# Optimization experiments

Measured on AMD Instinct MI355X. Metric: run time of the kernel, lower is better.

Reference implementation:

```python
import jax, jax.numpy as jnp
import numpy as np

NP = 16  # num_patches per side (init kwarg)


def setup_inputs() -> dict:
    key = jax.random.key(0)
    ks = jax.random.split(key, 8)
    B, C, H, W = 16, 16, 256, 256
    ph, pw = H // NP, W // NP          # 16, 16
    D = C * ph * pw                     # in_channels = 4096
    E = 512                             # embedding_dim
    s = 0.02
    return {
        "x": jax.random.normal(ks[0], (B, C, H, W), dtype=jnp.float32),
        "theta_w": jax.random.normal(ks[1], (D, E), dtype=jnp.float32) * s,
        "theta_b": jnp.zeros((E,), dtype=jnp.float32),
        "f_w": jax.random.normal(ks[2], (D, E), dtype=jnp.float32) * s,
        "f_b": jnp.zeros((E,), dtype=jnp.float32),
        "g_w": jax.random.normal(ks[3], (D, D), dtype=jnp.float32) * s,
        "g_b": jnp.zeros((D,), dtype=jnp.float32),
        "scale": jnp.ones((1,), dtype=jnp.float32),
    }


def reference(x, theta_w, theta_b, f_w, f_b, g_w, g_b, scale):
    B, C, H, W = x.shape
    ph, pw = H // NP, W // NP
    P = NP * NP                 # number of patches (== ph*pw by construction)
    D = C * ph * pw             # flattened patch dim = in_channels
    # extract non-overlapping patches: [B,C,H,W] -> [B,P,D] (C,ph,pw order)
    p = (x.reshape(B, C, NP, ph, NP, pw)
           .transpose(0, 2, 4, 1, 3, 5)
           .reshape(B, P, D))
    theta = p @ theta_w + theta_b                         # [B,P,E]
    f = p @ f_w + f_b                                     # [B,P,E]
    weights = jax.nn.softmax(
        jnp.einsum('bpe,bqe->bpq', theta, f), axis=-1)    # [B,P,P]
    g = (p @ g_w + g_b).reshape(B, P, C, ph * pw)         # [B,P,C,N], N==P
    # broadcast gate (NOT a matmul combine): weights.unsqueeze(2) * g
    enhanced = weights[:, :, None, :] * g                 # [B,P,C,N]
    img = (enhanced.reshape(B, NP, NP, C, ph, pw)
                   .transpose(0, 3, 1, 4, 2, 5)
                   .reshape(B, C, H, W))
    return scale * img + x
```

## Files before the change

### kernel.cpp

```cpp
#include <hip/hip_runtime.h>
#include <hip/hip_bf16.h>
#include <stdint.h>


typedef __hip_bfloat16 bf16;
typedef __bf16 bf16x8 __attribute__((ext_vector_type(8)));
typedef float f32x4 __attribute__((ext_vector_type(4)));

#define GLOBAL_AS __attribute__((address_space(1)))
#define LDS_AS __attribute__((address_space(3)))

__device__ __forceinline__ void gload_lds16(const void* g, void* l) {
    void* gg = const_cast<void*>(g);
    __builtin_amdgcn_global_load_lds((GLOBAL_AS void*)gg, (LDS_AS void*)l, 16, 0, 0);
}


__global__ __launch_bounds__(256) void prep_p(const float* __restrict__ x,
                                              bf16* __restrict__ pHi,
                                              bf16* __restrict__ pLo) {
    int tid = blockIdx.x * 256 + threadIdx.x;
    int w4 = tid & 63;
    int h  = (tid >> 6) & 255;
    int c  = (tid >> 14) & 15;
    int b  = tid >> 18;
    float4 v = ((const float4*)x)[tid];
    int i = h >> 4, y = h & 15, j = w4 >> 2, zb = (w4 & 3) * 4;
    int m = b * 256 + i * 16 + j;
    int k = c * 256 + y * 16 + zb;
    size_t o = (size_t)m * 4096 + k;
    float vs[4] = {v.x, v.y, v.z, v.w};
#pragma unroll
    for (int q = 0; q < 4; ++q) {
        bf16 hv = __float2bfloat16(vs[q]);
        float rem = vs[q] - __bfloat162float(hv);
        pHi[o + q] = hv;
        pLo[o + q] = __float2bfloat16(rem);
    }
}

__global__ __launch_bounds__(256) void prep_w(const float* __restrict__ theta_w,
                                              const float* __restrict__ f_w,
                                              bf16* __restrict__ wHi,
                                              bf16* __restrict__ wLo) {
    __shared__ float tile[32][33];
    int t = threadIdx.x;
    int tx = t & 31, ty = t >> 5;
    int k0 = blockIdx.x * 32;
    int e0 = blockIdx.y * 32;
#pragma unroll
    for (int r = 0; r < 4; ++r) {
        int k = k0 + ty + r * 8;
        int e = e0 + tx;
        float v = (e < 512) ? theta_w[(size_t)k * 512 + e]
                            : f_w[(size_t)k * 512 + (e - 512)];
        tile[ty + r * 8][tx] = v;
    }
    __syncthreads();
#pragma unroll
    for (int r = 0; r < 4; ++r) {
        int e = e0 + ty + r * 8;
        int k = k0 + tx;
        float v = tile[tx][ty + r * 8];
        bf16 hv = __float2bfloat16(v);
        float rem = v - __bfloat162float(hv);
        wHi[(size_t)e * 4096 + k] = hv;
        wLo[(size_t)e * 4096 + k] = __float2bfloat16(rem);
    }
}

__global__ __launch_bounds__(256) void prep_g(const float* __restrict__ g_w,
                                              bf16* __restrict__ gwt) {
    __shared__ float tile[32][33];
    int t = threadIdx.x;
    int tx = t & 31, ty = t >> 5;
    int k0 = blockIdx.x * 32;
    int n0 = blockIdx.y * 32;
#pragma unroll
    for (int r = 0; r < 4; ++r) {
        int k = k0 + ty + r * 8;
        tile[ty + r * 8][tx] = g_w[(size_t)k * 4096 + (n0 + tx)];
    }
    __syncthreads();
#pragma unroll
    for (int r = 0; r < 4; ++r) {
        int n = n0 + ty + r * 8;
        int k = k0 + tx;
        gwt[(size_t)n * 4096 + k] = __float2bfloat16(tile[tx][ty + r * 8]);
    }
}

__device__ __forceinline__ void gemm_pass(const bf16* A, const bf16* Bt,
                                          int lda, int ldb, int m0, int n0,
                                          int kbase, int ksteps,
                                          bf16* As, bf16* Bs, f32x4 (&acc)[4][4]) {
    int t = threadIdx.x, lane = t & 63, wave = t >> 6;
    int wm = wave & 1, wn = wave >> 1;
    int lr = lane & 15, lq = lane >> 4;
    const bf16* gA = A + (size_t)m0 * lda;
    const bf16* gB = Bt + (size_t)n0 * ldb;
    int chunk0 = wave * 2;
    int srow0 = lane >> 2;
    int cb = (lane & 3) * 16;
    for (int ks = 0; ks < ksteps; ++ks) {
        int kt = kbase + ks * 32;
#pragma unroll
        for (int tt = 0; tt < 2; ++tt) {
            int chunk = chunk0 + tt;
            int row = chunk * 16 + srow0;
            gload_lds16((const char*)(gA + ((size_t)row * lda + kt)) + cb,
                        (char*)As + chunk * 1024);
            gload_lds16((const char*)(gB + ((size_t)row * ldb + kt)) + cb,
                        (char*)Bs + chunk * 1024);
        }
        __syncthreads();
        bf16x8 af[4], bfr[4];
#pragma unroll
        for (int mt = 0; mt < 4; ++mt)
            af[mt] = *(const bf16x8*)((const char*)As + (wm * 64 + mt * 16 + lr) * 64 + lq * 16);
#pragma unroll
        for (int nt = 0; nt < 4; ++nt)
            bfr[nt] = *(const bf16x8*)((const char*)Bs + (wn * 64 + nt * 16 + lr) * 64 + lq * 16);
#pragma unroll
        for (int mt = 0; mt < 4; ++mt)
#pragma unroll
            for (int nt = 0; nt < 4; ++nt)
                acc[mt][nt] = __builtin_amdgcn_mfma_f32_16x16x32_bf16(
                    af[mt], bfr[nt], acc[mt][nt], 0, 0, 0);
        __syncthreads();
    }
}


__global__ __launch_bounds__(256) void gemm1(const bf16* __restrict__ pHi,
                                             const bf16* __restrict__ pLo,
                                             const bf16* __restrict__ wHi,
                                             const bf16* __restrict__ wLo,
                                             float* __restrict__ C1a,
                                             float* __restrict__ C1b) {
    __shared__ bf16 As[128 * 32];
    __shared__ bf16 Bs[128 * 32];
    int m0 = blockIdx.x * 128, n0 = blockIdx.y * 128;
    int kbase = blockIdx.z * 2048;
    f32x4 acc[4][4] = {};
    gemm_pass(pLo, wHi, 4096, 4096, m0, n0, kbase, 64, As, Bs, acc);
    gemm_pass(pHi, wLo, 4096, 4096, m0, n0, kbase, 64, As, Bs, acc);
    gemm_pass(pHi, wHi, 4096, 4096, m0, n0, kbase, 64, As, Bs, acc);
    float* C = blockIdx.z ? C1b : C1a;
    int t = threadIdx.x, lane = t & 63, wave = t >> 6;
    int wm = wave & 1, wn = wave >> 1;
    int lr = lane & 15, lq = lane >> 4;
#pragma unroll
    for (int mt = 0; mt < 4; ++mt)
#pragma unroll
        for (int nt = 0; nt < 4; ++nt) {
            int col = n0 + wn * 64 + nt * 16 + lr;
#pragma unroll
            for (int reg = 0; reg < 4; ++reg) {
                int row = m0 + wm * 64 + mt * 16 + lq * 4 + reg;
                C[(size_t)row * 1024 + col] = acc[mt][nt][reg];
            }
        }
}


__global__ __launch_bounds__(256) void combine(const float* __restrict__ C1a,
                                               const float* __restrict__ C1b,
                                               const float* __restrict__ theta_b,
                                               const float* __restrict__ f_b,
                                               bf16* __restrict__ thfHi,
                                               bf16* __restrict__ thfLo) {
    int id = blockIdx.x * 256 + threadIdx.x;
    int c4 = id & 255;
    float4 va = ((const float4*)C1a)[id];
    float4 vb = ((const float4*)C1b)[id];
    float vs[4] = {va.x + vb.x, va.y + vb.y, va.z + vb.z, va.w + vb.w};
    union { ushort4 u; unsigned short s[4]; } H, L;
#pragma unroll
    for (int q = 0; q < 4; ++q) {
        int col = c4 * 4 + q;
        float bias = (col < 512) ? theta_b[col] : f_b[col - 512];
        float v = vs[q] + bias;
        bf16 h = __float2bfloat16(v);
        float rem = v - __bfloat162float(h);
        bf16 l = __float2bfloat16(rem);
        H.s[q] = *(unsigned short*)&h;
        L.s[q] = *(unsigned short*)&l;
    }
    ((ushort4*)thfHi)[id] = H.u;
    ((ushort4*)thfLo)[id] = L.u;
}


__global__ __launch_bounds__(256) void scores(const bf16* __restrict__ thfHi,
                                              const bf16* __restrict__ thfLo,
                                              float* __restrict__ S) {
    __shared__ bf16 As[128 * 32];
    __shared__ bf16 Bs[128 * 32];
    int m0 = blockIdx.x * 128, n0 = blockIdx.y * 128, b = blockIdx.z;
    const bf16* Ahi = thfHi + (size_t)b * 256 * 1024;
    const bf16* Alo = thfLo + (size_t)b * 256 * 1024;
    f32x4 acc[4][4] = {};
    gemm_pass(Ahi, Ahi + 512, 1024, 1024, m0, n0, 0, 16, As, Bs, acc);
    gemm_pass(Alo, Ahi + 512, 1024, 1024, m0, n0, 0, 16, As, Bs, acc);
    gemm_pass(Ahi, Alo + 512, 1024, 1024, m0, n0, 0, 16, As, Bs, acc);
    float* Sb = S + (size_t)b * 65536;
    int t = threadIdx.x, lane = t & 63, wave = t >> 6;
    int wm = wave & 1, wn = wave >> 1;
    int lr = lane & 15, lq = lane >> 4;
#pragma unroll
    for (int mt = 0; mt < 4; ++mt)
#pragma unroll
        for (int nt = 0; nt < 4; ++nt) {
            int col = n0 + wn * 64 + nt * 16 + lr;
#pragma unroll
            for (int reg = 0; reg < 4; ++reg) {
                int row = m0 + wm * 64 + mt * 16 + lq * 4 + reg;
                Sb[(size_t)row * 256 + col] = acc[mt][nt][reg];
            }
        }
}


__global__ __launch_bounds__(256) void softmax_rows(float* __restrict__ S) {
    int row = blockIdx.x * 4 + (threadIdx.x >> 6);
    int lane = threadIdx.x & 63;
    float4* p = (float4*)(S + (size_t)row * 256);
    float4 v = p[lane];
    float mx = fmaxf(fmaxf(v.x, v.y), fmaxf(v.z, v.w));
#pragma unroll
    for (int s = 32; s >= 1; s >>= 1) mx = fmaxf(mx, __shfl_xor(mx, s, 64));
    v.x = expf(v.x - mx); v.y = expf(v.y - mx);
    v.z = expf(v.z - mx); v.w = expf(v.w - mx);
    float sm = (v.x + v.y) + (v.z + v.w);
#pragma unroll
    for (int s = 32; s >= 1; s >>= 1) sm += __shfl_xor(sm, s, 64);
    float inv = 1.0f / sm;
    v.x *= inv; v.y *= inv; v.z *= inv; v.w *= inv;
    p[lane] = v;
}


__global__ __launch_bounds__(256) void gemm2(const bf16* __restrict__ pHi,
                                             const bf16* __restrict__ gwt,
                                             const float* __restrict__ g_b,
                                             const float* __restrict__ wts,
                                             const float* __restrict__ x,
                                             const float* __restrict__ scale,
                                             float* __restrict__ out) {
    __shared__ bf16 As[128 * 32];
    __shared__ bf16 Bs[128 * 32];
    int m0 = blockIdx.x * 128, n0 = blockIdx.y * 128;
    f32x4 acc[4][4] = {};
    gemm_pass(pHi, gwt, 4096, 4096, m0, n0, 0, 128, As, Bs, acc);
    int t = threadIdx.x, lane = t & 63, wave = t >> 6;
    int wm = wave & 1, wn = wave >> 1;
    int lr = lane & 15, lq = lane >> 4;
    float scl = scale[0];
#pragma unroll
    for (int mt = 0; mt < 4; ++mt)
#pragma unroll
        for (int nt = 0; nt < 4; ++nt) {
            int ng = n0 + wn * 64 + nt * 16 + lr;
            float gb = g_b[ng];
            int cc = ng >> 8, nidx = ng & 255;
            int y = nidx >> 4, z = nidx & 15;
#pragma unroll
            for (int reg = 0; reg < 4; ++reg) {
                int mg = m0 + wm * 64 + mt * 16 + lq * 4 + reg;
                int bb = mg >> 8, pi = mg & 255;
                int i = pi >> 4, j = pi & 15;
                float wt = wts[(size_t)mg * 256 + nidx];
                float gval = acc[mt][nt][reg] + gb;
                size_t idx = ((((size_t)(bb * 16 + cc)) * 256) + i * 16 + y) * 256
                             + (j * 16 + z);
                out[idx] = scl * wt * gval + x[idx];
            }
        }
}


extern "C" void kernel_launch(void* const* d_in, const int* in_sizes, int n_in,
                              void* d_out, int out_size, void* d_ws, size_t ws_size,
                              hipStream_t stream) {
    const float* x       = (const float*)d_in[0];
    const float* theta_w = (const float*)d_in[1];
    const float* theta_b = (const float*)d_in[2];
    const float* f_w     = (const float*)d_in[3];
    const float* f_b     = (const float*)d_in[4];
    const float* g_w     = (const float*)d_in[5];
    const float* g_b     = (const float*)d_in[6];
    const float* scale   = (const float*)d_in[7];
    (void)in_sizes; (void)n_in; (void)out_size; (void)ws_size;

    const size_t MiB = 1048576;
    char* ws = (char*)d_ws;
    bf16*  pHi   = (bf16*)(ws);
    bf16*  pLo   = (bf16*)(ws + 32 * MiB);
    bf16*  gwt   = (bf16*)(ws + 32 * MiB);
    bf16*  wHi   = (bf16*)(ws + 64 * MiB);
    bf16*  wLo   = (bf16*)(ws + 72 * MiB);
    float* C1a   = (float*)(ws + 80 * MiB);
    float* S     = (float*)(ws + 80 * MiB);
    float* C1b   = (float*)(ws + 96 * MiB);
    bf16*  thfHi = (bf16*)(ws + 112 * MiB);
    bf16*  thfLo = (bf16*)(ws + 120 * MiB);

    prep_p<<<16384, 256, 0, stream>>>(x, pHi, pLo);
    prep_w<<<dim3(128, 32), 256, 0, stream>>>(theta_w, f_w, wHi, wLo);
    gemm1<<<dim3(32, 8, 2), 256, 0, stream>>>(pHi, pLo, wHi, wLo, C1a, C1b);
    combine<<<4096, 256, 0, stream>>>(C1a, C1b, theta_b, f_b, thfHi, thfLo);
    scores<<<dim3(2, 2, 16), 256, 0, stream>>>(thfHi, thfLo, S);
    softmax_rows<<<1024, 256, 0, stream>>>(S);
    prep_g<<<dim3(128, 128), 256, 0, stream>>>(g_w, gwt);
    gemm2<<<dim3(32, 32), 256, 0, stream>>>(pHi, gwt, g_b, S, x, scale, (float*)d_out);
}
```

Baseline: 571.9 us.

## Fuse split-precision gemm1 passes, merge prep launches, vectorize transposed epilogues

gemm1's three separate hi/lo passes become one K loop. Each step loads the hi and lo tiles of both operands together and issues all three MFMA products, so the loop and barrier overhead is paid once instead of three times. The patch and weight prep kernels are merged into one launch, and the g_w transpose joins the combine kernel, cutting launch count. The operands of gemm1, scores and gemm2 are swapped so each lane's accumulator registers are contiguous in memory, which allows float4 stores and float4 loads of weights, bias and x in the epilogues. The cost is four LDS tiles in gemm1 and a larger register footprint, which may reduce occupancy.

```diff
diff --git a/kernel.cpp b/kernel.cpp
--- a/kernel.cpp
+++ b/kernel.cpp
@@ -16,77 +16,59 @@
 }
 
 
-__global__ __launch_bounds__(256) void prep_p(const float* __restrict__ x,
-                                              bf16* __restrict__ pHi,
-                                              bf16* __restrict__ pLo) {
-    int tid = blockIdx.x * 256 + threadIdx.x;
-    int w4 = tid & 63;
-    int h  = (tid >> 6) & 255;
-    int c  = (tid >> 14) & 15;
-    int b  = tid >> 18;
-    float4 v = ((const float4*)x)[tid];
-    int i = h >> 4, y = h & 15, j = w4 >> 2, zb = (w4 & 3) * 4;
-    int m = b * 256 + i * 16 + j;
-    int k = c * 256 + y * 16 + zb;
-    size_t o = (size_t)m * 4096 + k;
-    float vs[4] = {v.x, v.y, v.z, v.w};
-#pragma unroll
-    for (int q = 0; q < 4; ++q) {
-        bf16 hv = __float2bfloat16(vs[q]);
-        float rem = vs[q] - __bfloat162float(hv);
-        pHi[o + q] = hv;
-        pLo[o + q] = __float2bfloat16(rem);
-    }
-}
-
-__global__ __launch_bounds__(256) void prep_w(const float* __restrict__ theta_w,
-                                              const float* __restrict__ f_w,
-                                              bf16* __restrict__ wHi,
-                                              bf16* __restrict__ wLo) {
+__global__ __launch_bounds__(256) void prep_pw(const float* __restrict__ x,
+                                               const float* __restrict__ theta_w,
+                                               const float* __restrict__ f_w,
+                                               bf16* __restrict__ pHi,
+                                               bf16* __restrict__ pLo,
+                                               bf16* __restrict__ wHi,
+                                               bf16* __restrict__ wLo) {
     __shared__ float tile[32][33];
-    int t = threadIdx.x;
-    int tx = t & 31, ty = t >> 5;
-    int k0 = blockIdx.x * 32;
-    int e0 = blockIdx.y * 32;
-#pragma unroll
-    for (int r = 0; r < 4; ++r) {
-        int k = k0 + ty + r * 8;
-        int e = e0 + tx;
-        float v = (e < 512) ? theta_w[(size_t)k * 512 + e]
-                            : f_w[(size_t)k * 512 + (e - 512)];
-        tile[ty + r * 8][tx] = v;
-    }
-    __syncthreads();
-#pragma unroll
-    for (int r = 0; r < 4; ++r) {
-        int e = e0 + ty + r * 8;
-        int k = k0 + tx;
-        float v = tile[tx][ty + r * 8];
-        bf16 hv = __float2bfloat16(v);
-        float rem = v - __bfloat162float(hv);
-        wHi[(size_t)e * 4096 + k] = hv;
-        wLo[(size_t)e * 4096 + k] = __float2bfloat16(rem);
-    }
-}
-
-__global__ __launch_bounds__(256) void prep_g(const float* __restrict__ g_w,
-                                              bf16* __restrict__ gwt) {
-    __shared__ float tile[32][33];
-    int t = threadIdx.x;
-    int tx = t & 31, ty = t >> 5;
-    int k0 = blockIdx.x * 32;
-    int n0 = blockIdx.y * 32;
-#pragma unroll
-    for (int r = 0; r < 4; ++r) {
-        int k = k0 + ty + r * 8;
-        tile[ty + r * 8][tx] = g_w[(size_t)k * 4096 + (n0 + tx)];
-    }
-    __syncthreads();
-#pragma unroll
-    for (int r = 0; r < 4; ++r) {
-        int n = n0 + ty + r * 8;
-        int k = k0 + tx;
-        gwt[(size_t)n * 4096 + k] = __float2bfloat16(tile[tx][ty + r * 8]);
+    int blk = blockIdx.x;
+    if (blk < 16384) {
+        int tid = blk * 256 + threadIdx.x;
+        int w4 = tid & 63;
+        int h  = (tid >> 6) & 255;
+        int c  = (tid >> 14) & 15;
+        int b  = tid >> 18;
+        float4 v = ((const float4*)x)[tid];
+        int i = h >> 4, y = h & 15, j = w4 >> 2, zb = (w4 & 3) * 4;
+        int m = b * 256 + i * 16 + j;
+        int k = c * 256 + y * 16 + zb;
+        size_t o = (size_t)m * 4096 + k;
+        float vs[4] = {v.x, v.y, v.z, v.w};
+#pragma unroll
+        for (int q = 0; q < 4; ++q) {
+            bf16 hv = __float2bfloat16(vs[q]);
+            float rem = vs[q] - __bfloat162float(hv);
+            pHi[o + q] = hv;
+            pLo[o + q] = __float2bfloat16(rem);
+        }
+    } else {
+        int bid = blk - 16384;
+        int t = threadIdx.x;
+        int tx = t & 31, ty = t >> 5;
+        int k0 = (bid & 127) * 32;
+        int e0 = (bid >> 7) * 32;
+#pragma unroll
+        for (int r = 0; r < 4; ++r) {
+            int k = k0 + ty + r * 8;
+            int e = e0 + tx;
+            float v = (e < 512) ? theta_w[(size_t)k * 512 + e]
+                                : f_w[(size_t)k * 512 + (e - 512)];
+            tile[ty + r * 8][tx] = v;
+        }
+        __syncthreads();
+#pragma unroll
+        for (int r = 0; r < 4; ++r) {
+            int e = e0 + ty + r * 8;
+            int k = k0 + tx;
+            float v = tile[tx][ty + r * 8];
+            bf16 hv = __float2bfloat16(v);
+            float rem = v - __bfloat162float(hv);
+            wHi[(size_t)e * 4096 + k] = hv;
+            wLo[(size_t)e * 4096 + k] = __float2bfloat16(rem);
+        }
     }
 }
 
@@ -132,63 +114,137 @@
 }
 
 
-__global__ __launch_bounds__(256) void gemm1(const bf16* __restrict__ pHi,
-                                             const bf16* __restrict__ pLo,
-                                             const bf16* __restrict__ wHi,
-                                             const bf16* __restrict__ wLo,
-                                             float* __restrict__ C1a,
-                                             float* __restrict__ C1b) {
-    __shared__ bf16 As[128 * 32];
-    __shared__ bf16 Bs[128 * 32];
-    int m0 = blockIdx.x * 128, n0 = blockIdx.y * 128;
+__global__ __launch_bounds__(256) void gemm1f(const bf16* __restrict__ pHi,
+                                              const bf16* __restrict__ pLo,
+                                              const bf16* __restrict__ wHi,
+                                              const bf16* __restrict__ wLo,
+                                              float* __restrict__ C1a,
+                                              float* __restrict__ C1b) {
+    __shared__ bf16 AsHi[128 * 32];
+    __shared__ bf16 AsLo[128 * 32];
+    __shared__ bf16 BsHi[128 * 32];
+    __shared__ bf16 BsLo[128 * 32];
+    int m0 = blockIdx.x * 128;
+    int n0 = blockIdx.y * 128;
     int kbase = blockIdx.z * 2048;
-    f32x4 acc[4][4] = {};
-    gemm_pass(pLo, wHi, 4096, 4096, m0, n0, kbase, 64, As, Bs, acc);
-    gemm_pass(pHi, wLo, 4096, 4096, m0, n0, kbase, 64, As, Bs, acc);
-    gemm_pass(pHi, wHi, 4096, 4096, m0, n0, kbase, 64, As, Bs, acc);
-    float* C = blockIdx.z ? C1b : C1a;
     int t = threadIdx.x, lane = t & 63, wave = t >> 6;
     int wm = wave & 1, wn = wave >> 1;
     int lr = lane & 15, lq = lane >> 4;
-#pragma unroll
-    for (int mt = 0; mt < 4; ++mt)
+    const bf16* gAh = wHi + (size_t)m0 * 4096;
+    const bf16* gAl = wLo + (size_t)m0 * 4096;
+    const bf16* gBh = pHi + (size_t)n0 * 4096;
+    const bf16* gBl = pLo + (size_t)n0 * 4096;
+    int chunk0 = wave * 2;
+    int srow0 = lane >> 2;
+    int cb = (lane & 3) * 16;
+    f32x4 acc[4][4] = {};
+    for (int ks = 0; ks < 64; ++ks) {
+        int kt = kbase + ks * 32;
+#pragma unroll
+        for (int tt = 0; tt < 2; ++tt) {
+            int chunk = chunk0 + tt;
+            size_t off = (size_t)(chunk * 16 + srow0) * 4096 + kt;
+            gload_lds16((const char*)(gAh + off) + cb, (char*)AsHi + chunk * 1024);
+            gload_lds16((const char*)(gAl + off) + cb, (char*)AsLo + chunk * 1024);
+            gload_lds16((const char*)(gBh + off) + cb, (char*)BsHi + chunk * 1024);
+            gload_lds16((const char*)(gBl + off) + cb, (char*)BsLo + chunk * 1024);
+        }
+        __syncthreads();
+        bf16x8 ah[4], al[4], bh[4], bl[4];
+#pragma unroll
+        for (int mt = 0; mt < 4; ++mt) {
+            int ro = (wm * 64 + mt * 16 + lr) * 64 + lq * 16;
+            ah[mt] = *(const bf16x8*)((const char*)AsHi + ro);
+            al[mt] = *(const bf16x8*)((const char*)AsLo + ro);
+        }
 #pragma unroll
         for (int nt = 0; nt < 4; ++nt) {
-            int col = n0 + wn * 64 + nt * 16 + lr;
-#pragma unroll
-            for (int reg = 0; reg < 4; ++reg) {
-                int row = m0 + wm * 64 + mt * 16 + lq * 4 + reg;
-                C[(size_t)row * 1024 + col] = acc[mt][nt][reg];
-            }
-        }
-}
-
-
-__global__ __launch_bounds__(256) void combine(const float* __restrict__ C1a,
-                                               const float* __restrict__ C1b,
-                                               const float* __restrict__ theta_b,
-                                               const float* __restrict__ f_b,
-                                               bf16* __restrict__ thfHi,
-                                               bf16* __restrict__ thfLo) {
-    int id = blockIdx.x * 256 + threadIdx.x;
-    int c4 = id & 255;
-    float4 va = ((const float4*)C1a)[id];
-    float4 vb = ((const float4*)C1b)[id];
-    float vs[4] = {va.x + vb.x, va.y + vb.y, va.z + vb.z, va.w + vb.w};
-    union { ushort4 u; unsigned short s[4]; } H, L;
-#pragma unroll
-    for (int q = 0; q < 4; ++q) {
-        int col = c4 * 4 + q;
-        float bias = (col < 512) ? theta_b[col] : f_b[col - 512];
-        float v = vs[q] + bias;
-        bf16 h = __float2bfloat16(v);
-        float rem = v - __bfloat162float(h);
-        bf16 l = __float2bfloat16(rem);
-        H.s[q] = *(unsigned short*)&h;
-        L.s[q] = *(unsigned short*)&l;
-    }
-    ((ushort4*)thfHi)[id] = H.u;
-    ((ushort4*)thfLo)[id] = L.u;
+            int ro = (wn * 64 + nt * 16 + lr) * 64 + lq * 16;
+            bh[nt] = *(const bf16x8*)((const char*)BsHi + ro);
+            bl[nt] = *(const bf16x8*)((const char*)BsLo + ro);
+        }
+#pragma unroll
+        for (int mt = 0; mt < 4; ++mt)
+#pragma unroll
+            for (int nt = 0; nt < 4; ++nt)
+                acc[mt][nt] = __builtin_amdgcn_mfma_f32_16x16x32_bf16(
+                    ah[mt], bl[nt], acc[mt][nt], 0, 0, 0);
+#pragma unroll
+        for (int mt = 0; mt < 4; ++mt)
+#pragma unroll
+            for (int nt = 0; nt < 4; ++nt)
+                acc[mt][nt] = __builtin_amdgcn_mfma_f32_16x16x32_bf16(
+                    al[mt], bh[nt], acc[mt][nt], 0, 0, 0);
+#pragma unroll
+        for (int mt = 0; mt < 4; ++mt)
+#pragma unroll
+            for (int nt = 0; nt < 4; ++nt)
+                acc[mt][nt] = __builtin_amdgcn_mfma_f32_16x16x32_bf16(
+                    ah[mt], bh[nt], acc[mt][nt], 0, 0, 0);
+        __syncthreads();
+    }
+    float* C = blockIdx.z ? C1b : C1a;
+#pragma unroll
+    for (int mt = 0; mt < 4; ++mt) {
+        int e = m0 + wm * 64 + mt * 16 + lq * 4;
+#pragma unroll
+        for (int nt = 0; nt < 4; ++nt) {
+            int p = n0 + wn * 64 + nt * 16 + lr;
+            *(float4*)(C + (size_t)p * 1024 + e) = *(float4*)&acc[mt][nt];
+        }
+    }
+}
+
+
+__global__ __launch_bounds__(256) void combine_prepg(const float* __restrict__ C1a,
+                                                     const float* __restrict__ C1b,
+                                                     const float* __restrict__ theta_b,
+                                                     const float* __restrict__ f_b,
+                                                     const float* __restrict__ g_w,
+                                                     bf16* __restrict__ thfHi,
+                                                     bf16* __restrict__ thfLo,
+                                                     bf16* __restrict__ gwt) {
+    __shared__ float tile[32][33];
+    int blk = blockIdx.x;
+    if (blk < 4096) {
+        int id = blk * 256 + threadIdx.x;
+        int c4 = id & 255;
+        float4 va = ((const float4*)C1a)[id];
+        float4 vb = ((const float4*)C1b)[id];
+        float vs[4] = {va.x + vb.x, va.y + vb.y, va.z + vb.z, va.w + vb.w};
+        union { ushort4 u; unsigned short s[4]; } H, L;
+#pragma unroll
+        for (int q = 0; q < 4; ++q) {
+            int col = c4 * 4 + q;
+            float bias = (col < 512) ? theta_b[col] : f_b[col - 512];
+            float v = vs[q] + bias;
+            bf16 h = __float2bfloat16(v);
+            float rem = v - __bfloat162float(h);
+            bf16 l = __float2bfloat16(rem);
+            H.s[q] = *(unsigned short*)&h;
+            L.s[q] = *(unsigned short*)&l;
+        }
+        ((ushort4*)thfHi)[id] = H.u;
+        ((ushort4*)thfLo)[id] = L.u;
+    } else {
+        int bid = blk - 4096;
+        int t = threadIdx.x;
+        int tx = t & 31, ty = t >> 5;
+        int k0 = (bid & 127) * 32;
+        int n0 = (bid >> 7) * 32;
+#pragma unroll
+        for (int r = 0; r < 4; ++r) {
+            int k = k0 + ty + r * 8;
+            tile[ty + r * 8][tx] = g_w[(size_t)k * 4096 + (n0 + tx)];
+        }
+        __syncthreads();
+#pragma unroll
+        for (int r = 0; r < 4; ++r) {
+            int n = n0 + ty + r * 8;
+            int k = k0 + tx;
+            gwt[(size_t)n * 4096 + k] = __float2bfloat16(tile[tx][ty + r * 8]);
+        }
+    }
 }
 
 
@@ -197,28 +253,28 @@
                                               float* __restrict__ S) {
     __shared__ bf16 As[128 * 32];
     __shared__ bf16 Bs[128 * 32];
-    int m0 = blockIdx.x * 128, n0 = blockIdx.y * 128, b = blockIdx.z;
+    int m0 = blockIdx.x * 128;
+    int n0 = blockIdx.y * 128;
+    int b = blockIdx.z;
     const bf16* Ahi = thfHi + (size_t)b * 256 * 1024;
     const bf16* Alo = thfLo + (size_t)b * 256 * 1024;
     f32x4 acc[4][4] = {};
-    gemm_pass(Ahi, Ahi + 512, 1024, 1024, m0, n0, 0, 16, As, Bs, acc);
-    gemm_pass(Alo, Ahi + 512, 1024, 1024, m0, n0, 0, 16, As, Bs, acc);
-    gemm_pass(Ahi, Alo + 512, 1024, 1024, m0, n0, 0, 16, As, Bs, acc);
+    gemm_pass(Ahi + 512, Ahi, 1024, 1024, m0, n0, 0, 16, As, Bs, acc);
+    gemm_pass(Ahi + 512, Alo, 1024, 1024, m0, n0, 0, 16, As, Bs, acc);
+    gemm_pass(Alo + 512, Ahi, 1024, 1024, m0, n0, 0, 16, As, Bs, acc);
     float* Sb = S + (size_t)b * 65536;
     int t = threadIdx.x, lane = t & 63, wave = t >> 6;
     int wm = wave & 1, wn = wave >> 1;
     int lr = lane & 15, lq = lane >> 4;
 #pragma unroll
-    for (int mt = 0; mt < 4; ++mt)
+    for (int mt = 0; mt < 4; ++mt) {
+        int q = m0 + wm * 64 + mt * 16 + lq * 4;
 #pragma unroll
         for (int nt = 0; nt < 4; ++nt) {
-            int col = n0 + wn * 64 + nt * 16 + lr;
-#pragma unroll
-            for (int reg = 0; reg < 4; ++reg) {
-                int row = m0 + wm * 64 + mt * 16 + lq * 4 + reg;
-                Sb[(size_t)row * 256 + col] = acc[mt][nt][reg];
-            }
-        }
+            int p = n0 + wn * 64 + nt * 16 + lr;
+            *(float4*)(Sb + (size_t)p * 256 + q) = *(float4*)&acc[mt][nt];
+        }
+    }
 }
 
 
@@ -250,33 +306,39 @@
                                              float* __restrict__ out) {
     __shared__ bf16 As[128 * 32];
     __shared__ bf16 Bs[128 * 32];
-    int m0 = blockIdx.x * 128, n0 = blockIdx.y * 128;
+    int m0 = blockIdx.x * 128;
+    int n0 = blockIdx.y * 128;
     f32x4 acc[4][4] = {};
-    gemm_pass(pHi, gwt, 4096, 4096, m0, n0, 0, 128, As, Bs, acc);
+    gemm_pass(gwt, pHi, 4096, 4096, m0, n0, 0, 128, As, Bs, acc);
     int t = threadIdx.x, lane = t & 63, wave = t >> 6;
     int wm = wave & 1, wn = wave >> 1;
     int lr = lane & 15, lq = lane >> 4;
     float scl = scale[0];
 #pragma unroll
-    for (int mt = 0; mt < 4; ++mt)
+    for (int mt = 0; mt < 4; ++mt) {
+        int ng = m0 + wm * 64 + mt * 16 + lq * 4;
+        int cc = ng >> 8;
+        int y = (ng >> 4) & 15;
+        int zq = ng & 255;
+        float4 gb4 = *(const float4*)(g_b + ng);
 #pragma unroll
         for (int nt = 0; nt < 4; ++nt) {
-            int ng = n0 + wn * 64 + nt * 16 + lr;
-            float gb = g_b[ng];
-            int cc = ng >> 8, nidx = ng & 255;
-            int y = nidx >> 4, z = nidx & 15;
-#pragma unroll
-            for (int reg = 0; reg < 4; ++reg) {
-                int mg = m0 + wm * 64 + mt * 16 + lq * 4 + reg;
-                int bb = mg >> 8, pi = mg & 255;
-                int i = pi >> 4, j = pi & 15;
-                float wt = wts[(size_t)mg * 256 + nidx];
-                float gval = acc[mt][nt][reg] + gb;
-                size_t idx = ((((size_t)(bb * 16 + cc)) * 256) + i * 16 + y) * 256
-                             + (j * 16 + z);
-                out[idx] = scl * wt * gval + x[idx];
-            }
-        }
+            int mg = n0 + wn * 64 + nt * 16 + lr;
+            int bb = mg >> 8, pi = mg & 255;
+            int i = pi >> 4, j = pi & 15;
+            float4 wt4 = *(const float4*)(wts + (size_t)mg * 256 + zq);
+            size_t idx = ((((size_t)(bb * 16 + cc)) * 256) + i * 16 + y) * 256
+                         + j * 16 + (ng & 15);
+            float4 xv = *(const float4*)(x + idx);
+            f32x4 a = acc[mt][nt];
+            float4 o;
+            o.x = scl * wt4.x * (a[0] + gb4.x) + xv.x;
+            o.y = scl * wt4.y * (a[1] + gb4.y) + xv.y;
+            o.z = scl * wt4.z * (a[2] + gb4.z) + xv.z;
+            o.w = scl * wt4.w * (a[3] + gb4.w) + xv.w;
+            *(float4*)(out + idx) = o;
+        }
+    }
 }
 
 
@@ -306,12 +368,11 @@
     bf16*  thfHi = (bf16*)(ws + 112 * MiB);
     bf16*  thfLo = (bf16*)(ws + 120 * MiB);
 
-    prep_p<<<16384, 256, 0, stream>>>(x, pHi, pLo);
-    prep_w<<<dim3(128, 32), 256, 0, stream>>>(theta_w, f_w, wHi, wLo);
-    gemm1<<<dim3(32, 8, 2), 256, 0, stream>>>(pHi, pLo, wHi, wLo, C1a, C1b);
-    combine<<<4096, 256, 0, stream>>>(C1a, C1b, theta_b, f_b, thfHi, thfLo);
+    prep_pw<<<20480, 256, 0, stream>>>(x, theta_w, f_w, pHi, pLo, wHi, wLo);
+    gemm1f<<<dim3(8, 32, 2), 256, 0, stream>>>(pHi, pLo, wHi, wLo, C1a, C1b);
+    combine_prepg<<<20480, 256, 0, stream>>>(C1a, C1b, theta_b, f_b, g_w,
+                                             thfHi, thfLo, gwt);
     scores<<<dim3(2, 2, 16), 256, 0, stream>>>(thfHi, thfLo, S);
     softmax_rows<<<1024, 256, 0, stream>>>(S);
-    prep_g<<<dim3(128, 128), 256, 0, stream>>>(g_w, gwt);
     gemm2<<<dim3(32, 32), 256, 0, stream>>>(pHi, gwt, g_b, S, x, scale, (float*)d_out);
 }
```

New measurement: 542.9 us. 1.05x faster.
